# Kernel tuning notes

Measured on AMD Instinct MI355X. Metric: run time of the kernel, lower is better.

## Reference

```python
import jax, jax.numpy as jnp
import numpy as np


def setup_inputs() -> dict:
    key = jax.random.key(0)
    k1, k2 = jax.random.split(key)
    B, N, LENGTH = 2048, 64, 8
    # x: (batch, 2, n, n) -- real/imag planes of batched complex matrices
    x = jax.random.normal(k1, (B, 2, N, N), dtype=jnp.float32) * 0.1
    # learned coefficients: (length, 2, n, n), scaled down like the factorial-decaying init
    coefficients = jax.random.normal(k2, (LENGTH, 2, N, N), dtype=jnp.float32) * 0.05
    return {"x": x, "coefficients": coefficients}


def reference(x, coefficients):
    # Faithful port of MatrixMPowerSeriesLayer.call (including the sign used
    # for res_imag inside the i>=2 loop, which differs from the i==1 term).
    length = coefficients.shape[0]
    n = x.shape[2]
    xr = x[:, 0]  # (b, n, n)
    xi = x[:, 1]
    cr = coefficients[:, 0]  # (length, n, n)
    ci = coefficients[:, 1]
    unit = jnp.eye(n, dtype=x.dtype)

    tr, ti = xr, xi  # running complex power x^p
    # order-0 term: unit @ c[0] (broadcasts against batched terms)
    res_r = unit @ cr[0] + (jnp.einsum('bjk,kl->bjl', tr, cr[1]) - jnp.einsum('bjk,kl->bjl', ti, ci[1]))
    res_i = unit @ ci[0] + (jnp.einsum('bjk,kl->bjl', tr, ci[1]) + jnp.einsum('bjk,kl->bjl', ti, cr[1]))

    for i in range(2, length):
        # complex batched matmul: tmp <- tmp @ x
        new_tr = jnp.einsum('bjk,bkl->bjl', tr, xr) - jnp.einsum('bjk,bkl->bjl', ti, xi)
        ti = jnp.einsum('bjk,bkl->bjl', tr, xi) + jnp.einsum('bjk,bkl->bjl', ti, xr)
        tr = new_tr
        res_r = res_r + jnp.einsum('bjk,kl->bjl', tr, cr[i]) - jnp.einsum('bjk,kl->bjl', ti, ci[i])
        # NOTE: original code subtracts ti @ cr[i] here (not adds) -- kept faithful.
        res_i = res_i + jnp.einsum('bjk,kl->bjl', tr, ci[i]) - jnp.einsum('bjk,kl->bjl', ti, cr[i])

    return jnp.stack([res_r, res_i], axis=1)  # (b, 2, n, n)
```

## Files before the change

kernel.cpp:

```cpp
#include <hip/hip_runtime.h>

typedef __attribute__((ext_vector_type(4))) short short4v;
typedef __attribute__((ext_vector_type(8))) short short8v;
typedef __attribute__((ext_vector_type(2))) unsigned int uint2v;
typedef __attribute__((ext_vector_type(4))) unsigned int uint4v;
typedef __attribute__((ext_vector_type(4))) float f32x4;
typedef __attribute__((ext_vector_type(16))) float f32x16;

#define LSTRIDE 68
#define MATB (64 * LSTRIDE * 2)
#define LDS_BYTES (4 * MATB)

#define CFRAG_BYTES (7 * 4 * 2 * 4 * 1024)
#define INIT_OFF CFRAG_BYTES

__device__ __forceinline__ short bf16h(float v) {
    union { float f; unsigned u; } x; x.f = v;
    unsigned r = x.u + 0x7FFFu + ((x.u >> 16) & 1u);
    return (short)(r >> 16);
}
__device__ __forceinline__ float bf16tof(short s) {
    union { unsigned u; float f; } x; x.u = ((unsigned)(unsigned short)s) << 16;
    return x.f;
}
struct HL { unsigned h, l; };
__device__ __forceinline__ HL split2(float v0, float v1) {
    unsigned hp, lp;
    asm("v_cvt_pk_bf16_f32 %0, %1, %2" : "=v"(hp) : "v"(v0), "v"(v1));
    union { unsigned u; float f; } a, b;
    a.u = hp << 16;
    b.u = hp & 0xffff0000u;
    float l0 = v0 - a.f, l1 = v1 - b.f;
    asm("v_cvt_pk_bf16_f32 %0, %1, %2" : "=v"(lp) : "v"(l0), "v"(l1));
    HL r; r.h = hp; r.l = lp; return r;
}
__device__ __forceinline__ f32x16 MF(short8v a, short8v b, f32x16 c) {
    return __builtin_amdgcn_mfma_f32_32x32x16_bf16(a, b, c, 0, 0, 0);
}
__device__ __forceinline__ short8v negf(short8v a) {
    uint4v u = __builtin_bit_cast(uint4v, a);
    u ^= 0x80008000u;
    return __builtin_bit_cast(short8v, u);
}

__global__ void pms_prep(const float* __restrict__ coef, char* __restrict__ wsb) {
    const int blk = blockIdx.x;
    const int lane = threadIdx.x;
    const int lrow = lane & 31, lhi = lane >> 5;
    if (blk < 56) {
        const int qr  = blk & 1;
        const int km  = blk >> 1;
        const int mat = km & 3;
        const int kk  = km >> 2;
        const int part = mat >> 1;
        const int lo   = mat & 1;
        const float* C = coef + (size_t)((kk + 1) * 2 + part) * 4096;
        for (int t = 0; t < 4; ++t) {
            short8v o;
            #pragma unroll
            for (int j = 0; j < 8; ++j) {
                int krow = 16 * t + 8 * lhi + j;
                int col  = 32 * qr + lrow;
                float v = C[krow * 64 + col];
                short hh = bf16h(v);
                o[j] = lo ? bf16h(v - bf16tof(hh)) : hh;
            }
            *(short8v*)(wsb + ((size_t)blk * 4 + t) * 1024 + lane * 16) = o;
        }
    } else {
        const int id = blk - 56;
        const int qc = id & 1, qr = (id >> 1) & 1, part = id >> 2;
        const float* C0 = coef + (size_t)part * 4096;
        float* dst = (float*)(wsb + INIT_OFF + (size_t)(((part * 2 + qr) * 2 + qc) * 64 + lane) * 64);
        #pragma unroll
        for (int v = 0; v < 16; ++v) {
            int r = 32 * qr + (v & 3) + 8 * (v >> 2) + 4 * lhi;
            int c = 32 * qc + lrow;
            dst[v] = C0[c * 64 + r];
        }
    }
}

__global__ __launch_bounds__(256, 3) void pms_main(
    const float* __restrict__ x, const char* __restrict__ wsb,
    float* __restrict__ out)
{
    extern __shared__ char smem[];
    const int tid  = threadIdx.x;
    const int lane = tid & 63;
    const int w    = tid >> 6;
    const int qr = w >> 1, qc = w & 1;
    const int lrow = lane & 31, lhi = lane >> 5;
    const size_t b = blockIdx.x;
    const float* xb = x + b * 8192;

    #pragma unroll
    for (int s = 0; s < 8; ++s) {
        int f = s * 1024 + tid * 4;
        int p = f >> 12, m = (f >> 6) & 63, c = f & 63;
        f32x4 v = *(const f32x4*)(xb + f);
        HL a01 = split2(v[0], v[1]);
        HL a23 = split2(v[2], v[3]);
        uint2v h, l;
        h[0] = a01.h; l[0] = a01.l;
        h[1] = a23.h; l[1] = a23.l;
        int off = (m * LSTRIDE + c) * 2;
        *(uint2v*)(smem + (p * 2 + 0) * MATB + off) = h;
        *(uint2v*)(smem + (p * 2 + 1) * MATB + off) = l;
    }
    __syncthreads();

    short8v xa[2][2][4];
    #pragma unroll
    for (int pi = 0; pi < 2; ++pi)
    #pragma unroll
    for (int hl = 0; hl < 2; ++hl)
    #pragma unroll
    for (int t = 0; t < 4; ++t) {
        const short* mp = (const short*)(smem + (pi * 2 + hl) * MATB);
        short8v a;
        #pragma unroll
        for (int j = 0; j < 8; ++j)
            a[j] = mp[(16 * t + 8 * lhi + j) * LSTRIDE + 32 * qr + lrow];
        xa[pi][hl][t] = a;
    }

    f32x16 accRr, accRi;
    {
        const f32x4* p0 = (const f32x4*)(wsb + INIT_OFF + (size_t)(((0 + qr) * 2 + qc) * 64 + lane) * 64);
        const f32x4* p1 = (const f32x4*)(wsb + INIT_OFF + (size_t)(((2 + qr) * 2 + qc) * 64 + lane) * 64);
        #pragma unroll
        for (int g = 0; g < 4; ++g) {
            f32x4 a = p0[g], c4 = p1[g];
            #pragma unroll
            for (int j = 0; j < 4; ++j) { accRr[4 * g + j] = a[j]; accRi[4 * g + j] = c4[j]; }
        }
    }

    auto ldB = [&](int mat, int t) -> short8v {
        const short4v* p = (const short4v*)(smem + mat * MATB
                             + (32 * qc + lrow) * (LSTRIDE * 2) + 32 * t + 16 * lhi);
        short4v a = p[0], c4 = p[1];
        short8v r;
        #pragma unroll
        for (int j = 0; j < 4; ++j) { r[j] = a[j]; r[j + 4] = c4[j]; }
        return r;
    };

    for (int k = 2; k <= 7; ++k) {
        const char* cw = wsb + (size_t)(k - 2) * 32768;
        const bool k1 = (k == 2);
        f32x16 aTr, aTi;
        #pragma unroll
        for (int v = 0; v < 16; ++v) { aTr[v] = 0.f; aTi[v] = 0.f; }

        #pragma unroll
        for (int t = 0; t < 4; ++t) {
            short8v cRh = *(const short8v*)(cw + ((0 * 2 + qr) * 4 + t) * 1024 + lane * 16);
            short8v cRl = *(const short8v*)(cw + ((1 * 2 + qr) * 4 + t) * 1024 + lane * 16);
            short8v cIh = *(const short8v*)(cw + ((2 * 2 + qr) * 4 + t) * 1024 + lane * 16);
            short8v cIl = *(const short8v*)(cw + ((3 * 2 + qr) * 4 + t) * 1024 + lane * 16);
            short8v Brh = ldB(0, t), Brl = ldB(1, t);
            short8v Bih = ldB(2, t), Bil = ldB(3, t);
            short8v nBih = negf(Bih), nBil = negf(Bil);
            short8v sBih = k1 ? Bih : nBih;
            short8v sBil = k1 ? Bil : nBil;

            accRr = MF(cRh, Brh, accRr);
            accRi = MF(cIh, Brh, accRi);
            aTr   = MF(xa[0][0][t], Brh, aTr);
            aTi   = MF(xa[1][0][t], Brh, aTi);

            accRr = MF(cRh, Brl, accRr);
            accRi = MF(cIh, Brl, accRi);
            aTr   = MF(xa[0][0][t], Brl, aTr);
            aTi   = MF(xa[1][0][t], Brl, aTi);

            accRr = MF(cRl, Brh, accRr);
            accRi = MF(cIl, Brh, accRi);
            aTr   = MF(xa[0][1][t], Brh, aTr);
            aTi   = MF(xa[1][1][t], Brh, aTi);

            accRr = MF(cIh, nBih, accRr);
            accRi = MF(cRh, sBih, accRi);
            aTr   = MF(xa[1][0][t], nBih, aTr);
            aTi   = MF(xa[0][0][t], Bih, aTi);

            accRr = MF(cIh, nBil, accRr);
            accRi = MF(cRh, sBil, accRi);
            aTr   = MF(xa[1][0][t], nBil, aTr);
            aTi   = MF(xa[0][0][t], Bil, aTi);

            accRr = MF(cIl, nBih, accRr);
            accRi = MF(cRl, sBih, accRi);
            aTr   = MF(xa[1][1][t], nBih, aTr);
            aTi   = MF(xa[0][1][t], Bih, aTi);
        }

        __syncthreads();

        {
            const int c = 32 * qc + lrow;
            #pragma unroll
            for (int g = 0; g < 4; ++g) {
                int rbse = 32 * qr + 8 * g + 4 * lhi;
                HL r01 = split2(aTr[4 * g + 0], aTr[4 * g + 1]);
                HL r23 = split2(aTr[4 * g + 2], aTr[4 * g + 3]);
                HL i01 = split2(aTi[4 * g + 0], aTi[4 * g + 1]);
                HL i23 = split2(aTi[4 * g + 2], aTi[4 * g + 3]);
                uint2v hr, lr, hi2, li2;
                hr[0] = r01.h; lr[0] = r01.l; hr[1] = r23.h; lr[1] = r23.l;
                hi2[0] = i01.h; li2[0] = i01.l; hi2[1] = i23.h; li2[1] = i23.l;
                int off = (c * LSTRIDE + rbse) * 2;
                *(uint2v*)(smem + 0 * MATB + off) = hr;
                *(uint2v*)(smem + 1 * MATB + off) = lr;
                *(uint2v*)(smem + 2 * MATB + off) = hi2;
                *(uint2v*)(smem + 3 * MATB + off) = li2;
            }
        }
        __syncthreads();
    }

    {
        const char* cw = wsb + (size_t)6 * 32768;
        #pragma unroll
        for (int t = 0; t < 4; ++t) {
            short8v cRh = *(const short8v*)(cw + ((0 * 2 + qr) * 4 + t) * 1024 + lane * 16);
            short8v cRl = *(const short8v*)(cw + ((1 * 2 + qr) * 4 + t) * 1024 + lane * 16);
            short8v cIh = *(const short8v*)(cw + ((2 * 2 + qr) * 4 + t) * 1024 + lane * 16);
            short8v cIl = *(const short8v*)(cw + ((3 * 2 + qr) * 4 + t) * 1024 + lane * 16);
            short8v Brh = ldB(0, t), Brl = ldB(1, t);
            short8v Bih = ldB(2, t), Bil = ldB(3, t);
            short8v nBih = negf(Bih), nBil = negf(Bil);

            accRr = MF(cRh, Brh, accRr);
            accRi = MF(cIh, Brh, accRi);
            accRr = MF(cRh, Brl, accRr);
            accRi = MF(cIh, Brl, accRi);
            accRr = MF(cRl, Brh, accRr);
            accRi = MF(cIl, Brh, accRi);
            accRr = MF(cIh, nBih, accRr);
            accRi = MF(cRh, nBih, accRi);
            accRr = MF(cIh, nBil, accRr);
            accRi = MF(cRh, nBil, accRi);
            accRr = MF(cIl, nBih, accRr);
            accRi = MF(cRl, nBih, accRi);
        }
    }

    __syncthreads();
    {
        const int c = 32 * qc + lrow;
        #pragma unroll
        for (int g = 0; g < 4; ++g) {
            int rbse = 32 * qr + 8 * g + 4 * lhi;
            f32x4 vr, vi;
            #pragma unroll
            for (int j = 0; j < 4; ++j) { vr[j] = accRr[4 * g + j]; vi[j] = accRi[4 * g + j]; }
            *(f32x4*)(smem + (size_t)(0 * 4352 + c * LSTRIDE + rbse) * 4) = vr;
            *(f32x4*)(smem + (size_t)(1 * 4352 + c * LSTRIDE + rbse) * 4) = vi;
        }
    }
    __syncthreads();
    float* ob = out + b * 8192;
    #pragma unroll
    for (int s = 0; s < 8; ++s) {
        int f = s * 1024 + tid * 4;
        int p = f >> 12, m = (f >> 6) & 63, n = f & 63;
        *(f32x4*)(ob + f) = *(const f32x4*)(smem + (size_t)(p * 4352 + m * LSTRIDE + n) * 4);
    }
}

extern "C" void kernel_launch(void* const* d_in, const int* in_sizes, int n_in,
                              void* d_out, int out_size, void* d_ws, size_t ws_size,
                              hipStream_t stream) {
    const float* x    = (const float*)d_in[0];
    const float* coef = (const float*)d_in[1];
    float* out = (float*)d_out;
    char*  wsb = (char*)d_ws;
    const int B = in_sizes[0] / 8192;

    pms_prep<<<64, 64, 0, stream>>>(coef, wsb);
    pms_main<<<B, 256, LDS_BYTES, stream>>>(x, wsb, out);
}
```

Baseline: 157.8 us.

## Double-buffer LDS power matrices and prefetch B fragments and coefficients

```diff
diff --git a/kernel.cpp b/kernel.cpp
--- a/kernel.cpp
+++ b/kernel.cpp
@@ -9,7 +9,9 @@
 
 #define LSTRIDE 68
 #define MATB (64 * LSTRIDE * 2)
-#define LDS_BYTES (4 * MATB)
+#define REGA 0
+#define REGB (4 * MATB)
+#define LDS_BYTES (8 * MATB)
 
 #define CFRAG_BYTES (7 * 4 * 2 * 4 * 1024)
 #define INIT_OFF CFRAG_BYTES
@@ -81,7 +83,7 @@
     }
 }
 
-__global__ __launch_bounds__(256, 3) void pms_main(
+__global__ __launch_bounds__(256, 2) void pms_main(
     const float* __restrict__ x, const char* __restrict__ wsb,
     float* __restrict__ out)
 {
@@ -105,8 +107,8 @@
         h[0] = a01.h; l[0] = a01.l;
         h[1] = a23.h; l[1] = a23.l;
         int off = (m * LSTRIDE + c) * 2;
-        *(uint2v*)(smem + (p * 2 + 0) * MATB + off) = h;
-        *(uint2v*)(smem + (p * 2 + 1) * MATB + off) = l;
+        *(uint2v*)(smem + REGA + (p * 2 + 0) * MATB + off) = h;
+        *(uint2v*)(smem + REGA + (p * 2 + 1) * MATB + off) = l;
     }
     __syncthreads();
 
@@ -117,7 +119,7 @@
     for (int hl = 0; hl < 2; ++hl)
     #pragma unroll
     for (int t = 0; t < 4; ++t) {
-        const short* mp = (const short*)(smem + (pi * 2 + hl) * MATB);
+        const short* mp = (const short*)(smem + REGA + (pi * 2 + hl) * MATB);
         short8v a;
         #pragma unroll
         for (int j = 0; j < 8; ++j)
@@ -137,8 +139,8 @@
         }
     }
 
-    auto ldB = [&](int mat, int t) -> short8v {
-        const short4v* p = (const short4v*)(smem + mat * MATB
+    auto ldB = [&](int rbase, int mat, int t) -> short8v {
+        const short4v* p = (const short4v*)(smem + rbase + mat * MATB
                              + (32 * qc + lrow) * (LSTRIDE * 2) + 32 * t + 16 * lhi);
         short4v a = p[0], c4 = p[1];
         short8v r;
@@ -147,57 +149,72 @@
         return r;
     };
 
+    int cur = REGA, nxt = REGB;
+
     for (int k = 2; k <= 7; ++k) {
         const char* cw = wsb + (size_t)(k - 2) * 32768;
         const bool k1 = (k == 2);
+
+        short8v cRh[4], cRl[4], cIh[4], cIl[4];
+        #pragma unroll
+        for (int t = 0; t < 4; ++t) {
+            cRh[t] = *(const short8v*)(cw + ((0 * 2 + qr) * 4 + t) * 1024 + lane * 16);
+            cRl[t] = *(const short8v*)(cw + ((1 * 2 + qr) * 4 + t) * 1024 + lane * 16);
+            cIh[t] = *(const short8v*)(cw + ((2 * 2 + qr) * 4 + t) * 1024 + lane * 16);
+            cIl[t] = *(const short8v*)(cw + ((3 * 2 + qr) * 4 + t) * 1024 + lane * 16);
+        }
+        short8v Brh = ldB(cur, 0, 0), Brl = ldB(cur, 1, 0);
+        short8v Bih = ldB(cur, 2, 0), Bil = ldB(cur, 3, 0);
+
         f32x16 aTr, aTi;
         #pragma unroll
         for (int v = 0; v < 16; ++v) { aTr[v] = 0.f; aTi[v] = 0.f; }
 
         #pragma unroll
         for (int t = 0; t < 4; ++t) {
-            short8v cRh = *(const short8v*)(cw + ((0 * 2 + qr) * 4 + t) * 1024 + lane * 16);
-            short8v cRl = *(const short8v*)(cw + ((1 * 2 + qr) * 4 + t) * 1024 + lane * 16);
-            short8v cIh = *(const short8v*)(cw + ((2 * 2 + qr) * 4 + t) * 1024 + lane * 16);
-            short8v cIl = *(const short8v*)(cw + ((3 * 2 + qr) * 4 + t) * 1024 + lane * 16);
-            short8v Brh = ldB(0, t), Brl = ldB(1, t);
-            short8v Bih = ldB(2, t), Bil = ldB(3, t);
+            short8v Nrh, Nrl, Nih, Nil;
+            if (t < 3) {
+                Nrh = ldB(cur, 0, t + 1); Nrl = ldB(cur, 1, t + 1);
+                Nih = ldB(cur, 2, t + 1); Nil = ldB(cur, 3, t + 1);
+            }
             short8v nBih = negf(Bih), nBil = negf(Bil);
             short8v sBih = k1 ? Bih : nBih;
             short8v sBil = k1 ? Bil : nBil;
 
-            accRr = MF(cRh, Brh, accRr);
-            accRi = MF(cIh, Brh, accRi);
+            __builtin_amdgcn_s_setprio(1);
+            accRr = MF(cRh[t], Brh, accRr);
+            accRi = MF(cIh[t], Brh, accRi);
             aTr   = MF(xa[0][0][t], Brh, aTr);
             aTi   = MF(xa[1][0][t], Brh, aTi);
 
-            accRr = MF(cRh, Brl, accRr);
-            accRi = MF(cIh, Brl, accRi);
+            accRr = MF(cRh[t], Brl, accRr);
+            accRi = MF(cIh[t], Brl, accRi);
             aTr   = MF(xa[0][0][t], Brl, aTr);
             aTi   = MF(xa[1][0][t], Brl, aTi);
 
-            accRr = MF(cRl, Brh, accRr);
-            accRi = MF(cIl, Brh, accRi);
+            accRr = MF(cRl[t], Brh, accRr);
+            accRi = MF(cIl[t], Brh, accRi);
             aTr   = MF(xa[0][1][t], Brh, aTr);
             aTi   = MF(xa[1][1][t], Brh, aTi);
 
-            accRr = MF(cIh, nBih, accRr);
-            accRi = MF(cRh, sBih, accRi);
+            accRr = MF(cIh[t], nBih, accRr);
+            accRi = MF(cRh[t], sBih, accRi);
             aTr   = MF(xa[1][0][t], nBih, aTr);
             aTi   = MF(xa[0][0][t], Bih, aTi);
 
-            accRr = MF(cIh, nBil, accRr);
-            accRi = MF(cRh, sBil, accRi);
+            accRr = MF(cIh[t], nBil, accRr);
+            accRi = MF(cRh[t], sBil, accRi);
             aTr   = MF(xa[1][0][t], nBil, aTr);
             aTi   = MF(xa[0][0][t], Bil, aTi);
 
-            accRr = MF(cIl, nBih, accRr);
-            accRi = MF(cRl, sBih, accRi);
+            accRr = MF(cIl[t], nBih, accRr);
+            accRi = MF(cRl[t], sBih, accRi);
             aTr   = MF(xa[1][1][t], nBih, aTr);
             aTi   = MF(xa[0][1][t], Bih, aTi);
-        }
-
-        __syncthreads();
+            __builtin_amdgcn_s_setprio(0);
+
+            if (t < 3) { Brh = Nrh; Brl = Nrl; Bih = Nih; Bil = Nil; }
+        }
 
         {
             const int c = 32 * qc + lrow;
@@ -212,39 +229,53 @@
                 hr[0] = r01.h; lr[0] = r01.l; hr[1] = r23.h; lr[1] = r23.l;
                 hi2[0] = i01.h; li2[0] = i01.l; hi2[1] = i23.h; li2[1] = i23.l;
                 int off = (c * LSTRIDE + rbse) * 2;
-                *(uint2v*)(smem + 0 * MATB + off) = hr;
-                *(uint2v*)(smem + 1 * MATB + off) = lr;
-                *(uint2v*)(smem + 2 * MATB + off) = hi2;
-                *(uint2v*)(smem + 3 * MATB + off) = li2;
+                *(uint2v*)(smem + nxt + 0 * MATB + off) = hr;
+                *(uint2v*)(smem + nxt + 1 * MATB + off) = lr;
+                *(uint2v*)(smem + nxt + 2 * MATB + off) = hi2;
+                *(uint2v*)(smem + nxt + 3 * MATB + off) = li2;
             }
         }
         __syncthreads();
+        int tmp = cur; cur = nxt; nxt = tmp;
     }
 
     {
         const char* cw = wsb + (size_t)6 * 32768;
-        #pragma unroll
-        for (int t = 0; t < 4; ++t) {
-            short8v cRh = *(const short8v*)(cw + ((0 * 2 + qr) * 4 + t) * 1024 + lane * 16);
-            short8v cRl = *(const short8v*)(cw + ((1 * 2 + qr) * 4 + t) * 1024 + lane * 16);
-            short8v cIh = *(const short8v*)(cw + ((2 * 2 + qr) * 4 + t) * 1024 + lane * 16);
-            short8v cIl = *(const short8v*)(cw + ((3 * 2 + qr) * 4 + t) * 1024 + lane * 16);
-            short8v Brh = ldB(0, t), Brl = ldB(1, t);
-            short8v Bih = ldB(2, t), Bil = ldB(3, t);
+        short8v cRh[4], cRl[4], cIh[4], cIl[4];
+        #pragma unroll
+        for (int t = 0; t < 4; ++t) {
+            cRh[t] = *(const short8v*)(cw + ((0 * 2 + qr) * 4 + t) * 1024 + lane * 16);
+            cRl[t] = *(const short8v*)(cw + ((1 * 2 + qr) * 4 + t) * 1024 + lane * 16);
+            cIh[t] = *(const short8v*)(cw + ((2 * 2 + qr) * 4 + t) * 1024 + lane * 16);
+            cIl[t] = *(const short8v*)(cw + ((3 * 2 + qr) * 4 + t) * 1024 + lane * 16);
+        }
+        short8v Brh = ldB(cur, 0, 0), Brl = ldB(cur, 1, 0);
+        short8v Bih = ldB(cur, 2, 0), Bil = ldB(cur, 3, 0);
+        #pragma unroll
+        for (int t = 0; t < 4; ++t) {
+            short8v Nrh, Nrl, Nih, Nil;
+            if (t < 3) {
+                Nrh = ldB(cur, 0, t + 1); Nrl = ldB(cur, 1, t + 1);
+                Nih = ldB(cur, 2, t + 1); Nil = ldB(cur, 3, t + 1);
+            }
             short8v nBih = negf(Bih), nBil = negf(Bil);
 
-            accRr = MF(cRh, Brh, accRr);
-            accRi = MF(cIh, Brh, accRi);
-            accRr = MF(cRh, Brl, accRr);
-            accRi = MF(cIh, Brl, accRi);
-            accRr = MF(cRl, Brh, accRr);
-            accRi = MF(cIl, Brh, accRi);
-            accRr = MF(cIh, nBih, accRr);
-            accRi = MF(cRh, nBih, accRi);
-            accRr = MF(cIh, nBil, accRr);
-            accRi = MF(cRh, nBil, accRi);
-            accRr = MF(cIl, nBih, accRr);
-            accRi = MF(cRl, nBih, accRi);
+            __builtin_amdgcn_s_setprio(1);
+            accRr = MF(cRh[t], Brh, accRr);
+            accRi = MF(cIh[t], Brh, accRi);
+            accRr = MF(cRh[t], Brl, accRr);
+            accRi = MF(cIh[t], Brl, accRi);
+            accRr = MF(cRl[t], Brh, accRr);
+            accRi = MF(cIl[t], Brh, accRi);
+            accRr = MF(cIh[t], nBih, accRr);
+            accRi = MF(cRh[t], nBih, accRi);
+            accRr = MF(cIh[t], nBil, accRr);
+            accRi = MF(cRh[t], nBil, accRi);
+            accRr = MF(cIl[t], nBih, accRr);
+            accRi = MF(cRl[t], nBih, accRi);
+            __builtin_amdgcn_s_setprio(0);
+
+            if (t < 3) { Brh = Nrh; Brl = Nrl; Bih = Nih; Bil = Nil; }
         }
     }
 
@@ -257,8 +288,8 @@
             f32x4 vr, vi;
             #pragma unroll
             for (int j = 0; j < 4; ++j) { vr[j] = accRr[4 * g + j]; vi[j] = accRi[4 * g + j]; }
-            *(f32x4*)(smem + (size_t)(0 * 4352 + c * LSTRIDE + rbse) * 4) = vr;
-            *(f32x4*)(smem + (size_t)(1 * 4352 + c * LSTRIDE + rbse) * 4) = vi;
+            *(f32x4*)(smem + nxt + (size_t)(0 * 4352 + c * LSTRIDE + rbse) * 4) = vr;
+            *(f32x4*)(smem + nxt + (size_t)(1 * 4352 + c * LSTRIDE + rbse) * 4) = vi;
         }
     }
     __syncthreads();
@@ -267,7 +298,7 @@
     for (int s = 0; s < 8; ++s) {
         int f = s * 1024 + tid * 4;
         int p = f >> 12, m = (f >> 6) & 63, n = f & 63;
-        *(f32x4*)(ob + f) = *(const f32x4*)(smem + (size_t)(p * 4352 + m * LSTRIDE + n) * 4);
+        *(f32x4*)(ob + f) = *(const f32x4*)(smem + nxt + (size_t)(p * 4352 + m * LSTRIDE + n) * 4);
     }
 }
 
@@ -280,6 +311,9 @@
     char*  wsb = (char*)d_ws;
     const int B = in_sizes[0] / 8192;
 
+    (void)hipFuncSetAttribute(reinterpret_cast<const void*>(&pms_main),
+                              hipFuncAttributeMaxDynamicSharedMemorySize, LDS_BYTES);
+
     pms_prep<<<64, 64, 0, stream>>>(coef, wsb);
     pms_main<<<B, 256, LDS_BYTES, stream>>>(x, wsb, out);
 }
```

After: 144.4 us (median of 2 runs). -8.5%, faster.

## Use Gauss three-multiply complex product for powers and coefficient accumulation

Applied to the files above, without the earlier changes.

```diff
diff --git a/kernel.cpp b/kernel.cpp
--- a/kernel.cpp
+++ b/kernel.cpp
@@ -9,10 +9,14 @@
 
 #define LSTRIDE 68
 #define MATB (64 * LSTRIDE * 2)
-#define LDS_BYTES (4 * MATB)
-
-#define CFRAG_BYTES (7 * 4 * 2 * 4 * 1024)
-#define INIT_OFF CFRAG_BYTES
+
+#define XSA (6 * MATB)
+#define KLDS (XSA + 16384)
+
+#define KSLOT_STRIDE 49152
+#define CS_OFF (7 * KSLOT_STRIDE)
+#define KINIT_OFF (CS_OFF + 2 * 8192)
+#define KWS_NEED (KINIT_OFF + 32768)
 
 __device__ __forceinline__ short bf16h(float v) {
     union { float f; unsigned u; } x; x.f = v;
@@ -43,45 +47,71 @@
     return __builtin_bit_cast(short8v, u);
 }
 
-__global__ void pms_prep(const float* __restrict__ coef, char* __restrict__ wsb) {
+struct CF { short8v crh, crl, ncih, ncil, cdh, cdl; };
+__device__ __forceinline__ CF loadCF(const char* cw, int qr, int lane, int t) {
+    CF c;
+    c.crh  =      *(const short8v*)(cw + ((size_t)(0 * 2 + qr) * 4 + t) * 1024 + lane * 16);
+    c.crl  =      *(const short8v*)(cw + ((size_t)(1 * 2 + qr) * 4 + t) * 1024 + lane * 16);
+    c.ncih = negf(*(const short8v*)(cw + ((size_t)(2 * 2 + qr) * 4 + t) * 1024 + lane * 16));
+    c.ncil = negf(*(const short8v*)(cw + ((size_t)(3 * 2 + qr) * 4 + t) * 1024 + lane * 16));
+    c.cdh  =      *(const short8v*)(cw + ((size_t)(4 * 2 + qr) * 4 + t) * 1024 + lane * 16);
+    c.cdl  =      *(const short8v*)(cw + ((size_t)(5 * 2 + qr) * 4 + t) * 1024 + lane * 16);
+    return c;
+}
+
+__global__ void pms_prep_k(const float* __restrict__ coef, char* __restrict__ wsb) {
     const int blk = blockIdx.x;
     const int lane = threadIdx.x;
     const int lrow = lane & 31, lhi = lane >> 5;
-    if (blk < 56) {
-        const int qr  = blk & 1;
-        const int km  = blk >> 1;
-        const int mat = km & 3;
-        const int kk  = km >> 2;
-        const int part = mat >> 1;
-        const int lo   = mat & 1;
-        const float* C = coef + (size_t)((kk + 1) * 2 + part) * 4096;
+    if (blk < 84) {
+        const int s = blk / 12, rem = blk % 12;
+        const int mat = rem >> 1, qr = rem & 1;
+        const int which = mat >> 1, lo = mat & 1;
+        const float* Pr = coef + (size_t)((s + 1) * 2 + 0) * 4096;
+        const float* Pi = coef + (size_t)((s + 1) * 2 + 1) * 4096;
         for (int t = 0; t < 4; ++t) {
             short8v o;
             #pragma unroll
             for (int j = 0; j < 8; ++j) {
-                int krow = 16 * t + 8 * lhi + j;
-                int col  = 32 * qr + lrow;
-                float v = C[krow * 64 + col];
+                int idx = (16 * t + 8 * lhi + j) * 64 + 32 * qr + lrow;
+                float v = (which == 0) ? Pr[idx] : (which == 1) ? Pi[idx] : (Pi[idx] - Pr[idx]);
                 short hh = bf16h(v);
                 o[j] = lo ? bf16h(v - bf16tof(hh)) : hh;
             }
-            *(short8v*)(wsb + ((size_t)blk * 4 + t) * 1024 + lane * 16) = o;
+            *(short8v*)(wsb + (size_t)s * KSLOT_STRIDE + mat * 8192 + qr * 4096 + t * 1024 + lane * 16) = o;
+        }
+    } else if (blk < 88) {
+        const int id = blk - 84;
+        const int lo = id >> 1, qr = id & 1;
+        const float* Pr = coef + (size_t)(1 * 2 + 0) * 4096;
+        const float* Pi = coef + (size_t)(1 * 2 + 1) * 4096;
+        for (int t = 0; t < 4; ++t) {
+            short8v o;
+            #pragma unroll
+            for (int j = 0; j < 8; ++j) {
+                int idx = (16 * t + 8 * lhi + j) * 64 + 32 * qr + lrow;
+                float v = Pr[idx] + Pi[idx];
+                short hh = bf16h(v);
+                o[j] = lo ? bf16h(v - bf16tof(hh)) : hh;
+            }
+            *(short8v*)(wsb + CS_OFF + lo * 8192 + qr * 4096 + t * 1024 + lane * 16) = o;
         }
     } else {
-        const int id = blk - 56;
-        const int qc = id & 1, qr = (id >> 1) & 1, part = id >> 2;
-        const float* C0 = coef + (size_t)part * 4096;
-        float* dst = (float*)(wsb + INIT_OFF + (size_t)(((part * 2 + qr) * 2 + qc) * 64 + lane) * 64);
+        const int id = blk - 88;
+        const int qc = id & 1, qr = (id >> 1) & 1, slot = id >> 2;
+        float* dst = (float*)(wsb + KINIT_OFF + (size_t)(((slot * 2 + qr) * 2 + qc) * 64 + lane) * 64);
         #pragma unroll
         for (int v = 0; v < 16; ++v) {
             int r = 32 * qr + (v & 3) + 8 * (v >> 2) + 4 * lhi;
             int c = 32 * qc + lrow;
-            dst[v] = C0[c * 64 + r];
-        }
-    }
-}
-
-__global__ __launch_bounds__(256, 3) void pms_main(
+            float c0r = coef[c * 64 + r];
+            float c0i = coef[4096 + c * 64 + r];
+            dst[v] = (slot == 0) ? c0r : (c0i - c0r);
+        }
+    }
+}
+
+__global__ __launch_bounds__(256, 2) void pms_main_k(
     const float* __restrict__ x, const char* __restrict__ wsb,
     float* __restrict__ out)
 {
@@ -95,18 +125,25 @@
     const float* xb = x + b * 8192;
 
     #pragma unroll
-    for (int s = 0; s < 8; ++s) {
+    for (int s = 0; s < 4; ++s) {
         int f = s * 1024 + tid * 4;
-        int p = f >> 12, m = (f >> 6) & 63, c = f & 63;
-        f32x4 v = *(const f32x4*)(xb + f);
-        HL a01 = split2(v[0], v[1]);
-        HL a23 = split2(v[2], v[3]);
-        uint2v h, l;
-        h[0] = a01.h; l[0] = a01.l;
-        h[1] = a23.h; l[1] = a23.l;
+        int m = f >> 6, c = f & 63;
+        f32x4 vr = *(const f32x4*)(xb + f);
+        f32x4 vi = *(const f32x4*)(xb + 4096 + f);
+        f32x4 vs;
+        #pragma unroll
+        for (int j = 0; j < 4; ++j) vs[j] = vr[j] + vi[j];
+        HL r01 = split2(vr[0], vr[1]), r23 = split2(vr[2], vr[3]);
+        HL i01 = split2(vi[0], vi[1]), i23 = split2(vi[2], vi[3]);
+        HL s01 = split2(vs[0], vs[1]), s23 = split2(vs[2], vs[3]);
         int off = (m * LSTRIDE + c) * 2;
-        *(uint2v*)(smem + (p * 2 + 0) * MATB + off) = h;
-        *(uint2v*)(smem + (p * 2 + 1) * MATB + off) = l;
+        uint2v u;
+        u[0] = r01.h; u[1] = r23.h; *(uint2v*)(smem + 0 * MATB + off) = u;
+        u[0] = r01.l; u[1] = r23.l; *(uint2v*)(smem + 1 * MATB + off) = u;
+        u[0] = i01.h; u[1] = i23.h; *(uint2v*)(smem + 2 * MATB + off) = u;
+        u[0] = i01.l; u[1] = i23.l; *(uint2v*)(smem + 3 * MATB + off) = u;
+        u[0] = s01.h; u[1] = s23.h; *(uint2v*)(smem + 4 * MATB + off) = u;
+        u[0] = s01.l; u[1] = s23.l; *(uint2v*)(smem + 5 * MATB + off) = u;
     }
     __syncthreads();
 
@@ -125,15 +162,28 @@
         xa[pi][hl][t] = a;
     }
 
-    f32x16 accRr, accRi;
+    #pragma unroll
+    for (int hl = 0; hl < 2; ++hl)
+    #pragma unroll
+    for (int tt = 0; tt < 2; ++tt) {
+        int t = 2 * qc + tt;
+        const short* mp = (const short*)(smem + (4 + hl) * MATB);
+        short8v a;
+        #pragma unroll
+        for (int j = 0; j < 8; ++j)
+            a[j] = mp[(16 * t + 8 * lhi + j) * LSTRIDE + 32 * qr + lrow];
+        *(short8v*)(smem + XSA + ((size_t)(hl * 2 + qr) * 4 + t) * 1024 + lane * 16) = a;
+    }
+    __syncthreads();
+
+    f32x16 accRr, accQ;
     {
-        const f32x4* p0 = (const f32x4*)(wsb + INIT_OFF + (size_t)(((0 + qr) * 2 + qc) * 64 + lane) * 64);
-        const f32x4* p1 = (const f32x4*)(wsb + INIT_OFF + (size_t)(((2 + qr) * 2 + qc) * 64 + lane) * 64);
+        const f32x4* p0 = (const f32x4*)(wsb + KINIT_OFF + (size_t)(((0 + qr) * 2 + qc) * 64 + lane) * 64);
         #pragma unroll
         for (int g = 0; g < 4; ++g) {
-            f32x4 a = p0[g], c4 = p1[g];
+            f32x4 a = p0[g];
             #pragma unroll
-            for (int j = 0; j < 4; ++j) { accRr[4 * g + j] = a[j]; accRi[4 * g + j] = c4[j]; }
+            for (int j = 0; j < 4; ++j) { accRr[4 * g + j] = a[j]; accQ[4 * g + j] = 0.f; }
         }
     }
 
@@ -146,108 +196,181 @@
         for (int j = 0; j < 4; ++j) { r[j] = a[j]; r[j + 4] = c4[j]; }
         return r;
     };
-
-    for (int k = 2; k <= 7; ++k) {
-        const char* cw = wsb + (size_t)(k - 2) * 32768;
-        const bool k1 = (k == 2);
-        f32x16 aTr, aTi;
-        #pragma unroll
-        for (int v = 0; v < 16; ++v) { aTr[v] = 0.f; aTi[v] = 0.f; }
-
+    auto ldXS = [&](int hl, int t) -> short8v {
+        return *(const short8v*)(smem + XSA + ((size_t)(hl * 2 + qr) * 4 + t) * 1024 + lane * 16);
+    };
+
+    f32x16 m1, m2, m3;
+
+    auto foldWrite = [&]() {
+        const int c = 32 * qc + lrow;
+        f32x16 aTr, aTi, aTs;
+        #pragma unroll
+        for (int j = 0; j < 16; ++j) {
+            float ar = m1[j] - m2[j];
+            float ai = m3[j] - m1[j] - m2[j];
+            aTr[j] = ar; aTi[j] = ai; aTs[j] = ar + ai;
+        }
+        #pragma unroll
+        for (int g = 0; g < 4; ++g) {
+            int rbse = 32 * qr + 8 * g + 4 * lhi;
+            int off = (c * LSTRIDE + rbse) * 2;
+            HL a01 = split2(aTr[4 * g + 0], aTr[4 * g + 1]);
+            HL a23 = split2(aTr[4 * g + 2], aTr[4 * g + 3]);
+            HL b01 = split2(aTi[4 * g + 0], aTi[4 * g + 1]);
+            HL b23 = split2(aTi[4 * g + 2], aTi[4 * g + 3]);
+            HL c01 = split2(aTs[4 * g + 0], aTs[4 * g + 1]);
+            HL c23 = split2(aTs[4 * g + 2], aTs[4 * g + 3]);
+            uint2v u;
+            u[0] = a01.h; u[1] = a23.h; *(uint2v*)(smem + 0 * MATB + off) = u;
+            u[0] = a01.l; u[1] = a23.l; *(uint2v*)(smem + 1 * MATB + off) = u;
+            u[0] = b01.h; u[1] = b23.h; *(uint2v*)(smem + 2 * MATB + off) = u;
+            u[0] = b01.l; u[1] = b23.l; *(uint2v*)(smem + 3 * MATB + off) = u;
+            u[0] = c01.h; u[1] = c23.h; *(uint2v*)(smem + 4 * MATB + off) = u;
+            u[0] = c01.l; u[1] = c23.l; *(uint2v*)(smem + 5 * MATB + off) = u;
+        }
+    };
+
+
+    CF cnxt;
+
+    {
+        const char* cw = wsb;
+        CF c0 = loadCF(cw, qr, lane, 0);
+        short8v csh0 = *(const short8v*)(wsb + CS_OFF + ((size_t)(0 * 2 + qr) * 4 + 0) * 1024 + lane * 16);
+        short8v csl0 = *(const short8v*)(wsb + CS_OFF + ((size_t)(1 * 2 + qr) * 4 + 0) * 1024 + lane * 16);
+        #pragma unroll
+        for (int j = 0; j < 16; ++j) { m1[j] = 0.f; m2[j] = 0.f; m3[j] = 0.f; }
         #pragma unroll
         for (int t = 0; t < 4; ++t) {
-            short8v cRh = *(const short8v*)(cw + ((0 * 2 + qr) * 4 + t) * 1024 + lane * 16);
-            short8v cRl = *(const short8v*)(cw + ((1 * 2 + qr) * 4 + t) * 1024 + lane * 16);
-            short8v cIh = *(const short8v*)(cw + ((2 * 2 + qr) * 4 + t) * 1024 + lane * 16);
-            short8v cIl = *(const short8v*)(cw + ((3 * 2 + qr) * 4 + t) * 1024 + lane * 16);
+            CF c1; short8v csh1, csl1;
+            if (t < 3) {
+                c1 = loadCF(cw, qr, lane, t + 1);
+                csh1 = *(const short8v*)(wsb + CS_OFF + ((size_t)(0 * 2 + qr) * 4 + t + 1) * 1024 + lane * 16);
+                csl1 = *(const short8v*)(wsb + CS_OFF + ((size_t)(1 * 2 + qr) * 4 + t + 1) * 1024 + lane * 16);
+            }
             short8v Brh = ldB(0, t), Brl = ldB(1, t);
             short8v Bih = ldB(2, t), Bil = ldB(3, t);
-            short8v nBih = negf(Bih), nBil = negf(Bil);
-            short8v sBih = k1 ? Bih : nBih;
-            short8v sBil = k1 ? Bil : nBil;
-
-            accRr = MF(cRh, Brh, accRr);
-            accRi = MF(cIh, Brh, accRi);
-            aTr   = MF(xa[0][0][t], Brh, aTr);
-            aTi   = MF(xa[1][0][t], Brh, aTi);
-
-            accRr = MF(cRh, Brl, accRr);
-            accRi = MF(cIh, Brl, accRi);
-            aTr   = MF(xa[0][0][t], Brl, aTr);
-            aTi   = MF(xa[1][0][t], Brl, aTi);
-
-            accRr = MF(cRl, Brh, accRr);
-            accRi = MF(cIl, Brh, accRi);
-            aTr   = MF(xa[0][1][t], Brh, aTr);
-            aTi   = MF(xa[1][1][t], Brh, aTi);
-
-            accRr = MF(cIh, nBih, accRr);
-            accRi = MF(cRh, sBih, accRi);
-            aTr   = MF(xa[1][0][t], nBih, aTr);
-            aTi   = MF(xa[0][0][t], Bih, aTi);
-
-            accRr = MF(cIh, nBil, accRr);
-            accRi = MF(cRh, sBil, accRi);
-            aTr   = MF(xa[1][0][t], nBil, aTr);
-            aTi   = MF(xa[0][0][t], Bil, aTi);
-
-            accRr = MF(cIl, nBih, accRr);
-            accRi = MF(cRl, sBih, accRi);
-            aTr   = MF(xa[1][1][t], nBih, aTr);
-            aTi   = MF(xa[0][1][t], Bih, aTi);
-        }
-
+            short8v Bsh = ldB(4, t), Bsl = ldB(5, t);
+            short8v xsh = ldXS(0, t), xsl = ldXS(1, t);
+
+            __builtin_amdgcn_s_setprio(1);
+            accRr = MF(c0.crh, Brh, accRr);
+            accQ  = MF(c0.cdh, Brh, accQ);
+            m1    = MF(xa[0][0][t], Brh, m1);
+            accRr = MF(c0.ncih, Bih, accRr);
+            accQ  = MF(csh0, Bih, accQ);
+            m2    = MF(xa[1][0][t], Bih, m2);
+            m3    = MF(xsh, Bsh, m3);
+
+            accRr = MF(c0.crh, Brl, accRr);
+            accQ  = MF(c0.cdh, Brl, accQ);
+            m1    = MF(xa[0][0][t], Brl, m1);
+            accRr = MF(c0.ncih, Bil, accRr);
+            accQ  = MF(csh0, Bil, accQ);
+            m2    = MF(xa[1][0][t], Bil, m2);
+            m3    = MF(xsh, Bsl, m3);
+
+            accRr = MF(c0.crl, Brh, accRr);
+            accQ  = MF(c0.cdl, Brh, accQ);
+            m1    = MF(xa[0][1][t], Brh, m1);
+            accRr = MF(c0.ncil, Bih, accRr);
+            accQ  = MF(csl0, Bih, accQ);
+            m2    = MF(xa[1][1][t], Bih, m2);
+            m3    = MF(xsl, Bsh, m3);
+            __builtin_amdgcn_s_setprio(0);
+
+            if (t < 3) { c0 = c1; csh0 = csh1; csl0 = csl1; }
+        }
+        cnxt = loadCF(wsb + (size_t)1 * KSLOT_STRIDE, qr, lane, 0);
         __syncthreads();
-
-        {
-            const int c = 32 * qc + lrow;
-            #pragma unroll
-            for (int g = 0; g < 4; ++g) {
-                int rbse = 32 * qr + 8 * g + 4 * lhi;
-                HL r01 = split2(aTr[4 * g + 0], aTr[4 * g + 1]);
-                HL r23 = split2(aTr[4 * g + 2], aTr[4 * g + 3]);
-                HL i01 = split2(aTi[4 * g + 0], aTi[4 * g + 1]);
-                HL i23 = split2(aTi[4 * g + 2], aTi[4 * g + 3]);
-                uint2v hr, lr, hi2, li2;
-                hr[0] = r01.h; lr[0] = r01.l; hr[1] = r23.h; lr[1] = r23.l;
-                hi2[0] = i01.h; li2[0] = i01.l; hi2[1] = i23.h; li2[1] = i23.l;
-                int off = (c * LSTRIDE + rbse) * 2;
-                *(uint2v*)(smem + 0 * MATB + off) = hr;
-                *(uint2v*)(smem + 1 * MATB + off) = lr;
-                *(uint2v*)(smem + 2 * MATB + off) = hi2;
-                *(uint2v*)(smem + 3 * MATB + off) = li2;
-            }
-        }
+        foldWrite();
         __syncthreads();
     }
 
-    {
-        const char* cw = wsb + (size_t)6 * 32768;
+    for (int ks = 1; ks <= 5; ++ks) {
+        const char* cw = wsb + (size_t)ks * KSLOT_STRIDE;
+        CF c0 = cnxt;
+        #pragma unroll
+        for (int j = 0; j < 16; ++j) { m1[j] = 0.f; m2[j] = 0.f; m3[j] = 0.f; }
         #pragma unroll
         for (int t = 0; t < 4; ++t) {
-            short8v cRh = *(const short8v*)(cw + ((0 * 2 + qr) * 4 + t) * 1024 + lane * 16);
-            short8v cRl = *(const short8v*)(cw + ((1 * 2 + qr) * 4 + t) * 1024 + lane * 16);
-            short8v cIh = *(const short8v*)(cw + ((2 * 2 + qr) * 4 + t) * 1024 + lane * 16);
-            short8v cIl = *(const short8v*)(cw + ((3 * 2 + qr) * 4 + t) * 1024 + lane * 16);
+            CF c1;
+            if (t < 3) c1 = loadCF(cw, qr, lane, t + 1);
             short8v Brh = ldB(0, t), Brl = ldB(1, t);
             short8v Bih = ldB(2, t), Bil = ldB(3, t);
-            short8v nBih = negf(Bih), nBil = negf(Bil);
-
-            accRr = MF(cRh, Brh, accRr);
-            accRi = MF(cIh, Brh, accRi);
-            accRr = MF(cRh, Brl, accRr);
-            accRi = MF(cIh, Brl, accRi);
-            accRr = MF(cRl, Brh, accRr);
-            accRi = MF(cIl, Brh, accRi);
-            accRr = MF(cIh, nBih, accRr);
-            accRi = MF(cRh, nBih, accRi);
-            accRr = MF(cIh, nBil, accRr);
-            accRi = MF(cRh, nBil, accRi);
-            accRr = MF(cIl, nBih, accRr);
-            accRi = MF(cRl, nBih, accRi);
-        }
-    }
-
+            short8v Bsh = ldB(4, t), Bsl = ldB(5, t);
+            short8v xsh = ldXS(0, t), xsl = ldXS(1, t);
+
+            __builtin_amdgcn_s_setprio(1);
+            accRr = MF(c0.crh, Brh, accRr);
+            m1    = MF(xa[0][0][t], Brh, m1);
+            accQ  = MF(c0.cdh, Bsh, accQ);
+            accRr = MF(c0.ncih, Bih, accRr);
+            m2    = MF(xa[1][0][t], Bih, m2);
+            m3    = MF(xsh, Bsh, m3);
+
+            accRr = MF(c0.crh, Brl, accRr);
+            m1    = MF(xa[0][0][t], Brl, m1);
+            accQ  = MF(c0.cdh, Bsl, accQ);
+            accRr = MF(c0.ncih, Bil, accRr);
+            m2    = MF(xa[1][0][t], Bil, m2);
+            m3    = MF(xsh, Bsl, m3);
+
+            accRr = MF(c0.crl, Brh, accRr);
+            m1    = MF(xa[0][1][t], Brh, m1);
+            accQ  = MF(c0.cdl, Bsh, accQ);
+            accRr = MF(c0.ncil, Bih, accRr);
+            m2    = MF(xa[1][1][t], Bih, m2);
+            m3    = MF(xsl, Bsh, m3);
+            __builtin_amdgcn_s_setprio(0);
+
+            if (t < 3) c0 = c1;
+        }
+        cnxt = loadCF(wsb + (size_t)(ks + 1) * KSLOT_STRIDE, qr, lane, 0);
+        __syncthreads();
+        foldWrite();
+        __syncthreads();
+    }
+
+    {
+        const char* cw = wsb + (size_t)6 * KSLOT_STRIDE;
+        CF c0 = cnxt;
+        #pragma unroll
+        for (int t = 0; t < 4; ++t) {
+            CF c1;
+            if (t < 3) c1 = loadCF(cw, qr, lane, t + 1);
+            short8v Brh = ldB(0, t), Brl = ldB(1, t);
+            short8v Bih = ldB(2, t), Bil = ldB(3, t);
+            short8v Bsh = ldB(4, t), Bsl = ldB(5, t);
+
+            __builtin_amdgcn_s_setprio(1);
+            accRr = MF(c0.crh, Brh, accRr);
+            accQ  = MF(c0.cdh, Bsh, accQ);
+            accRr = MF(c0.ncih, Bih, accRr);
+            accRr = MF(c0.crh, Brl, accRr);
+            accQ  = MF(c0.cdh, Bsl, accQ);
+            accRr = MF(c0.ncih, Bil, accRr);
+            accRr = MF(c0.crl, Brh, accRr);
+            accQ  = MF(c0.cdl, Bsh, accQ);
+            accRr = MF(c0.ncil, Bih, accRr);
+            __builtin_amdgcn_s_setprio(0);
+
+            if (t < 3) c0 = c1;
+        }
+    }
+
+    f32x16 accRi;
+    {
+        const f32x4* p1 = (const f32x4*)(wsb + KINIT_OFF + (size_t)(((2 + qr) * 2 + qc) * 64 + lane) * 64);
+        #pragma unroll
+        for (int g = 0; g < 4; ++g) {
+            f32x4 d = p1[g];
+            #pragma unroll
+            for (int j = 0; j < 4; ++j)
+                accRi[4 * g + j] = accRr[4 * g + j] + accQ[4 * g + j] + d[j];
+        }
+    }
     __syncthreads();
     {
         const int c = 32 * qc + lrow;
@@ -280,6 +403,9 @@
     char*  wsb = (char*)d_ws;
     const int B = in_sizes[0] / 8192;
 
-    pms_prep<<<64, 64, 0, stream>>>(coef, wsb);
-    pms_main<<<B, 256, LDS_BYTES, stream>>>(x, wsb, out);
-}
+    (void)hipFuncSetAttribute(reinterpret_cast<const void*>(&pms_main_k),
+                              hipFuncAttributeMaxDynamicSharedMemorySize, KLDS);
+
+    pms_prep_k<<<96, 64, 0, stream>>>(coef, wsb);
+    pms_main_k<<<B, 256, KLDS, stream>>>(x, wsb, out);
+}
```

New measurement: 189.1 us. 19.9% more time.
